# Performance work log

Measured on AMD Instinct MI355X. Metric: run time of the kernel, lower is better.

## Reference

```python
import jax, jax.numpy as jnp
import numpy as np

N_NODES = 50000
N_EDGES = 1600000
IN_DIM = 128
HID = 64
N_GRAPHS = 256


def gcn_conv(x, row, col, W, b, n_nodes):
    """PyG GCNConv: symmetric gcn_norm with self-loops, linear-then-aggregate."""
    h = x @ W  # [N, out]
    loop = jnp.arange(n_nodes, dtype=row.dtype)
    r = jnp.concatenate([row, loop])  # sources (messages from x[r])
    c = jnp.concatenate([col, loop])  # targets (aggregate at c)
    ew = jnp.ones(r.shape[0], dtype=x.dtype)
    deg = jax.ops.segment_sum(ew, c, num_segments=n_nodes)
    dinv = jnp.where(deg > 0, jax.lax.rsqrt(deg), 0.0).astype(x.dtype)
    norm = dinv[r] * dinv[c]  # [E+N]
    out = jax.ops.segment_sum(norm[:, None] * h[r], c, num_segments=n_nodes)
    return out + b


def global_mean_pool(x, batch, n_graphs):
    sums = jax.ops.segment_sum(x, batch, num_segments=n_graphs)
    cnt = jax.ops.segment_sum(jnp.ones(x.shape[0], x.dtype), batch, num_segments=n_graphs)
    return sums / jnp.clip(cnt, 1.0)[:, None]


def setup_inputs() -> dict:
    key = jax.random.key(0)
    ks = jax.random.split(key, 12)
    x = jax.random.normal(ks[0], (N_NODES, IN_DIM), dtype=jnp.float32)
    edge_index = jax.random.randint(ks[1], (2, N_EDGES), 0, N_NODES, dtype=jnp.int64)
    batch = jnp.sort(jax.random.randint(ks[2], (N_NODES,), 0, N_GRAPHS, dtype=jnp.int64))
    def glorot(k, shp):
        lim = float(np.sqrt(6.0 / (shp[0] + shp[1])))
        return jax.random.uniform(k, shp, jnp.float32, -lim, lim)
    return {
        "x": x,
        "edge_index": edge_index,
        "batch": batch,
        "W1": glorot(ks[3], (IN_DIM, HID)), "b1": jnp.zeros((HID,), jnp.float32),
        "W2": glorot(ks[4], (HID, HID)), "b2": jnp.zeros((HID,), jnp.float32),
        "W3": glorot(ks[5], (HID, HID)), "b3": jnp.zeros((HID,), jnp.float32),
        "Wl1": glorot(ks[6], (HID, 16)), "bl1": jnp.zeros((16,), jnp.float32),
        "Wl2": glorot(ks[7], (16, 1)), "bl2": jnp.zeros((1,), jnp.float32),
    }


def reference(x, edge_index, batch, W1, b1, W2, b2, W3, b3, Wl1, bl1, Wl2, bl2):
    n = x.shape[0]
    row, col = edge_index[0], edge_index[1]
    h = jax.nn.relu(gcn_conv(x, row, col, W1, b1, n))
    h = jax.nn.relu(gcn_conv(h, row, col, W2, b2, n))
    h = jax.nn.relu(gcn_conv(h, row, col, W3, b3, n))
    g = global_mean_pool(h, batch, N_GRAPHS)  # [G, 64]
    out = (g @ Wl1 + bl1) @ Wl2 + bl2  # [G, 1]
    return out
```

## Files before the change

kernel.cpp:

```cpp
#include <hip/hip_runtime.h>

#define HID 64
#define B1 512
#define NBMAX 200
#define CAP 10368
#define ENTCAP 3200
#define CPT 21
#define QBITS 3

typedef __attribute__((ext_vector_type(8))) short short8;
typedef __attribute__((ext_vector_type(4))) float float4v;
typedef float f32x2 __attribute__((ext_vector_type(2)));

__device__ __forceinline__ ushort f2bf(float f) {
  unsigned u = __float_as_uint(f);
  unsigned r = (u + 0x7fffu + ((u >> 16) & 1u)) >> 16;
  return (ushort)r;
}
__device__ __forceinline__ float bf2f(ushort v) {
  return __uint_as_float(((unsigned)v) << 16);
}

__device__ __forceinline__ void acc8(f32x2& a01, f32x2& a23, uint2 d) {
  f32x2 t0, t1;
  t0.x = __uint_as_float(d.x << 16);
  t0.y = __uint_as_float(d.x & 0xffff0000u);
  t1.x = __uint_as_float(d.y << 16);
  t1.y = __uint_as_float(d.y & 0xffff0000u);
  a01 += t0;
  a23 += t1;
}


__global__ __launch_bounds__(256) void bucket_hist(const int* __restrict__ col, int E, int epb,
                                                   int* __restrict__ blockcnt,
                                                   const float* __restrict__ W1,
                                                   ushort* __restrict__ Wt1h,
                                                   ushort* __restrict__ Wt1l) {
  int b = blockIdx.x, t = threadIdx.x;
  int gt = b * 256 + t;
  if (gt < 128 * 64) {
    int k = gt >> 6, nn = gt & 63;
    float w = W1[gt];
    ushort h = f2bf(w);
    Wt1h[nn * 128 + k] = h;
    Wt1l[nn * 128 + k] = f2bf(w - bf2f(h));
  }

  __shared__ int cnt[256];
  cnt[t] = 0;
  __syncthreads();
  int lo = b * epb, hi = min(lo + epb, E);
  int ecnt = hi - lo;
  if (ecnt > 0) {
    int ecnt4 = ecnt & ~3;
    for (int i = t * 4; i < ecnt4; i += 1024) {
      int4 c4 = *(const int4*)&col[lo + i];
      atomicAdd(&cnt[c4.x >> 8], 1);
      atomicAdd(&cnt[c4.y >> 8], 1);
      atomicAdd(&cnt[c4.z >> 8], 1);
      atomicAdd(&cnt[c4.w >> 8], 1);
    }
    for (int i = ecnt4 + t; i < ecnt; i += 256) atomicAdd(&cnt[col[lo + i] >> 8], 1);
  }
  __syncthreads();
  blockcnt[b * 256 + t] = cnt[t];
}

__global__ __launch_bounds__(512) void scan_blocks(int* __restrict__ blockcnt,
                                                   int* __restrict__ buckettot) {
  __shared__ int s[512];
  int k = blockIdx.x;
  int t = threadIdx.x;
  int v = blockcnt[t * 256 + k];
  s[t] = v;
  __syncthreads();
  for (int d = 1; d < 512; d <<= 1) {
    int u = (t >= d) ? s[t - d] : 0;
    __syncthreads();
    s[t] += u;
    __syncthreads();
  }
  blockcnt[t * 256 + k] = s[t] - v;
  if (t == 511) buckettot[k] = s[t];
}

__global__ __launch_bounds__(256) void scan_buckettot(const int* __restrict__ buckettot,
                                                      int* __restrict__ bucketbase,
                                                      int* __restrict__ csr_off, int n, int E,
                                                      int nb) {
  __shared__ int s[256];
  int t = threadIdx.x;
  int v = buckettot[t];
  s[t] = v;
  __syncthreads();
  for (int d = 1; d < 256; d <<= 1) {
    int u = (t >= d) ? s[t - d] : 0;
    __syncthreads();
    s[t] += u;
    __syncthreads();
  }
  bucketbase[t] = s[t] - v;
  if (t == 255) bucketbase[256] = s[255];
  if (t == 0) csr_off[n] = E;
}

__global__ __launch_bounds__(256) void bin_edges(const int* __restrict__ row,
                                                 const int* __restrict__ col, int E, int epb,
                                                 const int* __restrict__ blockcnt,
                                                 const int* __restrict__ bucketbase,
                                                 unsigned* __restrict__ binned) {
  __shared__ int cnt[256];
  __shared__ int ofs[256];
  __shared__ int gb[256];
  __shared__ int lcur[256];
  __shared__ unsigned ent[ENTCAP];
  __shared__ unsigned stage[ENTCAP];
  int b = blockIdx.x, t = threadIdx.x;
  int lo = b * epb, hi = min(lo + epb, E);
  int ecnt = hi - lo;

  cnt[t] = 0;
  __syncthreads();
  if (ecnt > 0) {
    int ecnt4 = ecnt & ~3;
    for (int i = t * 4; i < ecnt4; i += 1024) {
      int4 c4 = *(const int4*)&col[lo + i];
      int4 r4 = *(const int4*)&row[lo + i];
      uint4 e4;
      e4.x = ((unsigned)r4.x << 16) | (unsigned)c4.x;
      e4.y = ((unsigned)r4.y << 16) | (unsigned)c4.y;
      e4.z = ((unsigned)r4.z << 16) | (unsigned)c4.z;
      e4.w = ((unsigned)r4.w << 16) | (unsigned)c4.w;
      *(uint4*)&ent[i] = e4;
      atomicAdd(&cnt[c4.x >> 8], 1);
      atomicAdd(&cnt[c4.y >> 8], 1);
      atomicAdd(&cnt[c4.z >> 8], 1);
      atomicAdd(&cnt[c4.w >> 8], 1);
    }
    for (int i = ecnt4 + t; i < ecnt; i += 256) {
      int c = col[lo + i];
      int r = row[lo + i];
      ent[i] = ((unsigned)r << 16) | (unsigned)c;
      atomicAdd(&cnt[c >> 8], 1);
    }
  }
  __syncthreads();
  int v = cnt[t];
  ofs[t] = v;
  __syncthreads();
  for (int d = 1; d < 256; d <<= 1) {
    int u = (t >= d) ? ofs[t - d] : 0;
    __syncthreads();
    ofs[t] += u;
    __syncthreads();
  }
  int excl = ofs[t] - v;
  int g = bucketbase[t] + blockcnt[b * 256 + t];
  __syncthreads();
  ofs[t] = excl;
  gb[t] = g;
  lcur[t] = excl;
  __syncthreads();
  if (ecnt > 0) {
    for (int i = t; i < ecnt; i += 256) {
      unsigned en = ent[i];
      int p = atomicAdd(&lcur[(en >> 8) & 255], 1);
      stage[p] = en;
    }
  }
  __syncthreads();
  if (ecnt > 0) {
    for (int i = t; i < ecnt; i += 256) {
      unsigned en = stage[i];
      int bb = (en >> 8) & 255;
      binned[gb[bb] + (i - ofs[bb])] = en;
    }
  }
}

__global__ __launch_bounds__(512) void bucket_csr(const unsigned* __restrict__ binned,
                                                  const int* __restrict__ bucketbase,
                                                  int* __restrict__ csr_off,
                                                  int* __restrict__ csr_src,
                                                  float* __restrict__ dinv, int n) {
  __shared__ int cnt[256 << QBITS];
  __shared__ int sscan[512];
  __shared__ int lsrc[CAP];
  int k = blockIdx.x, t = threadIdx.x;
  int base = bucketbase[k], end = bucketbase[k + 1];
  int s = end - base;
  unsigned ent[CPT];
  cnt[t] = 0; cnt[512 + t] = 0; cnt[1024 + t] = 0; cnt[1536 + t] = 0;
  __syncthreads();
#pragma unroll
  for (int q = 0; q < CPT; ++q) {
    int i = q * 512 + t;
    if (i < s) {
      unsigned p = binned[base + i];
      ent[q] = p;
      atomicAdd(&cnt[((p & 255u) << QBITS) | ((p >> 29) & 7u)], 1);
    }
  }
  __syncthreads();
  int a0 = cnt[t * 4 + 0], a1 = cnt[t * 4 + 1], a2 = cnt[t * 4 + 2], a3 = cnt[t * 4 + 3];
  int tsum = a0 + a1 + a2 + a3;
  sscan[t] = tsum;
  __syncthreads();
  for (int d = 1; d < 512; d <<= 1) {
    int u = (t >= d) ? sscan[t - d] : 0;
    __syncthreads();
    sscan[t] += u;
    __syncthreads();
  }
  int ex = sscan[t] - tsum;
  cnt[t * 4 + 0] = ex;
  cnt[t * 4 + 1] = ex + a0;
  cnt[t * 4 + 2] = ex + a0 + a1;
  cnt[t * 4 + 3] = ex + a0 + a1 + a2;
  __syncthreads();
  if (t < 256) {
    int st = cnt[t << QBITS];
    int en2 = (t == 255) ? s : cnt[(t + 1) << QBITS];
    int node = (k << 8) + t;
    if (node < n) {
      csr_off[node] = base + st;
      dinv[node] = rsqrtf((float)(en2 - st + 1));
    }
  }
  __syncthreads();
#pragma unroll
  for (int q = 0; q < CPT; ++q) {
    int i = q * 512 + t;
    if (i < s) {
      unsigned p = ent[q];
      int pos = atomicAdd(&cnt[((p & 255u) << QBITS) | ((p >> 29) & 7u)], 1);
      if (pos < CAP) lsrc[pos] = (int)(p >> 16);
    }
  }
  __syncthreads();
  for (int i = t; i < s; i += 512) csr_src[base + i] = (i < CAP) ? lsrc[i] : 0;
}


template <int K>
__global__ __launch_bounds__(256) void gemm_mfma(const float* __restrict__ A,
                                                 const ushort* __restrict__ Wh,
                                                 const ushort* __restrict__ Wl,
                                                 const float* __restrict__ dinv,
                                                 ushort* __restrict__ out, int n) {
  int wave = (blockIdx.x * 256 + threadIdx.x) >> 6;
  int lane = threadIdx.x & 63;
  int row0 = wave * 16;
  if (row0 >= n) return;
  int m = lane & 15;
  int quad = lane >> 4;
  int r = row0 + m;
  int rc = (r < n) ? r : (n - 1);

  float4v acc[4];
#pragma unroll
  for (int t = 0; t < 4; ++t) acc[t] = (float4v){0.f, 0.f, 0.f, 0.f};

#pragma unroll
  for (int k0 = 0; k0 < K; k0 += 32) {
    const float4* xp = (const float4*)&A[(size_t)rc * K + k0 + quad * 8];
    float4 a0 = xp[0];
    float4 a1 = xp[1];
    float av[8] = {a0.x, a0.y, a0.z, a0.w, a1.x, a1.y, a1.z, a1.w};
    short8 ah, al;
#pragma unroll
    for (int i = 0; i < 8; ++i) {
      ushort h = f2bf(av[i]);
      ah[i] = (short)h;
      al[i] = (short)f2bf(av[i] - bf2f(h));
    }
#pragma unroll
    for (int t = 0; t < 4; ++t) {
      size_t wof = (size_t)(t * 16 + m) * K + k0 + quad * 8;
      short8 bh = *(const short8*)&Wh[wof];
      short8 bl = *(const short8*)&Wl[wof];
      acc[t] = __builtin_amdgcn_mfma_f32_16x16x32_bf16(ah, bh, acc[t], 0, 0, 0);
      acc[t] = __builtin_amdgcn_mfma_f32_16x16x32_bf16(al, bh, acc[t], 0, 0, 0);
      acc[t] = __builtin_amdgcn_mfma_f32_16x16x32_bf16(ah, bl, acc[t], 0, 0, 0);
    }
  }

  float4 dv = ((const float4*)dinv)[(row0 >> 2) + quad];
  float dvi[4] = {dv.x, dv.y, dv.z, dv.w};
#pragma unroll
  for (int i = 0; i < 4; ++i) {
    int orow = row0 + quad * 4 + i;
    if (orow < n) {
#pragma unroll
      for (int t = 0; t < 4; ++t) {
        out[(size_t)orow * 64 + t * 16 + m] = f2bf(dvi[i] * acc[t][i]);
      }
    }
  }
}


__global__ __launch_bounds__(256) void agg_gemm(
    const ushort* __restrict__ hs_in, const int* __restrict__ csr_off,
    const int* __restrict__ csr_src, const float* __restrict__ dinv,
    const float* __restrict__ bias, const float* __restrict__ W,
    ushort* __restrict__ hs_out, int n) {
  int wid = (blockIdx.x * 256 + threadIdx.x) >> 6;
  int lane = threadIdx.x & 63;
  if (wid >= n) return;
  int qe = lane >> 4;
  int fq = lane & 15;
  const uint2* hs2 = (const uint2*)hs_in;

  f32x2 a01 = {0.f, 0.f}, a23 = {0.f, 0.f};
  if (qe == 0) {
    acc8(a01, a23, hs2[(size_t)wid * 16 + fq]);
  }

  int j = csr_off[wid];
  int e = csr_off[wid + 1];

  int pre = min(e, (j + 3) & ~3);
  if (j + qe < pre) {
    int s0 = csr_src[j + qe];
    acc8(a01, a23, hs2[(size_t)s0 * 16 + fq]);
  }
  int base = pre;

  for (; base + 16 <= e; base += 16) {
    int4 s = *(const int4*)&csr_src[base + qe * 4];
    uint2 v0 = hs2[(size_t)s.x * 16 + fq];
    uint2 v1 = hs2[(size_t)s.y * 16 + fq];
    uint2 v2 = hs2[(size_t)s.z * 16 + fq];
    uint2 v3 = hs2[(size_t)s.w * 16 + fq];
    acc8(a01, a23, v0);
    acc8(a01, a23, v1);
    acc8(a01, a23, v2);
    acc8(a01, a23, v3);
  }

  for (; base + 4 <= e; base += 4) {
    int s0 = csr_src[base + qe];
    acc8(a01, a23, hs2[(size_t)s0 * 16 + fq]);
  }
  if (base + qe < e) {
    int s0 = csr_src[base + qe];
    acc8(a01, a23, hs2[(size_t)s0 * 16 + fq]);
  }

  a01.x += __shfl_xor(a01.x, 16, 64);
  a01.y += __shfl_xor(a01.y, 16, 64);
  a23.x += __shfl_xor(a23.x, 16, 64);
  a23.y += __shfl_xor(a23.y, 16, 64);
  a01.x += __shfl_xor(a01.x, 32, 64);
  a01.y += __shfl_xor(a01.y, 32, 64);
  a23.x += __shfl_xor(a23.x, 32, 64);
  a23.y += __shfl_xor(a23.y, 32, 64);

  float dd = dinv[wid];
  float4 bi = ((const float4*)bias)[fq];
  float r0 = fmaxf(dd * a01.x + bi.x, 0.f);
  float r1 = fmaxf(dd * a01.y + bi.y, 0.f);
  float r2 = fmaxf(dd * a23.x + bi.z, 0.f);
  float r3 = fmaxf(dd * a23.y + bi.w, 0.f);

  float h0 = 0.f, h1 = 0.f, h2 = 0.f, h3 = 0.f;
#pragma unroll
  for (int kq = 0; kq < 16; ++kq) {
    float f0 = __shfl(r0, kq, 64);
    float f1 = __shfl(r1, kq, 64);
    float f2 = __shfl(r2, kq, 64);
    float f3 = __shfl(r3, kq, 64);
    h0 += f0 * W[(kq * 4 + 0) * 64 + lane];
    h1 += f1 * W[(kq * 4 + 1) * 64 + lane];
    h2 += f2 * W[(kq * 4 + 2) * 64 + lane];
    h3 += f3 * W[(kq * 4 + 3) * 64 + lane];
  }
  float h = (h0 + h1) + (h2 + h3);
  hs_out[(size_t)wid * 64 + lane] = f2bf(dd * h);
}


__global__ __launch_bounds__(256) void agg_kernel(
    const ushort* __restrict__ hs, const int* __restrict__ csr_off,
    const int* __restrict__ csr_src, const float* __restrict__ dinv,
    const float* __restrict__ bias, float* __restrict__ out, int n) {
  int wid = (blockIdx.x * 256 + threadIdx.x) >> 6;
  int lane = threadIdx.x & 63;
  if (wid >= n) return;
  int qe = lane >> 4;
  int fq = lane & 15;
  const uint2* hs2 = (const uint2*)hs;

  f32x2 a01 = {0.f, 0.f}, a23 = {0.f, 0.f};
  if (qe == 0) {
    acc8(a01, a23, hs2[(size_t)wid * 16 + fq]);
  }

  int j = csr_off[wid];
  int e = csr_off[wid + 1];

  int pre = min(e, (j + 3) & ~3);
  if (j + qe < pre) {
    int s0 = csr_src[j + qe];
    acc8(a01, a23, hs2[(size_t)s0 * 16 + fq]);
  }
  int base = pre;

  for (; base + 16 <= e; base += 16) {
    int4 s = *(const int4*)&csr_src[base + qe * 4];
    uint2 v0 = hs2[(size_t)s.x * 16 + fq];
    uint2 v1 = hs2[(size_t)s.y * 16 + fq];
    uint2 v2 = hs2[(size_t)s.z * 16 + fq];
    uint2 v3 = hs2[(size_t)s.w * 16 + fq];
    acc8(a01, a23, v0);
    acc8(a01, a23, v1);
    acc8(a01, a23, v2);
    acc8(a01, a23, v3);
  }

  for (; base + 4 <= e; base += 4) {
    int s0 = csr_src[base + qe];
    acc8(a01, a23, hs2[(size_t)s0 * 16 + fq]);
  }
  if (base + qe < e) {
    int s0 = csr_src[base + qe];
    acc8(a01, a23, hs2[(size_t)s0 * 16 + fq]);
  }

  a01.x += __shfl_xor(a01.x, 16, 64);
  a01.y += __shfl_xor(a01.y, 16, 64);
  a23.x += __shfl_xor(a23.x, 16, 64);
  a23.y += __shfl_xor(a23.y, 16, 64);
  a01.x += __shfl_xor(a01.x, 32, 64);
  a01.y += __shfl_xor(a01.y, 32, 64);
  a23.x += __shfl_xor(a23.x, 32, 64);
  a23.y += __shfl_xor(a23.y, 32, 64);

  if (qe == 0) {
    float d = dinv[wid];
    float4 bi = ((const float4*)bias)[fq];
    float4 r;
    r.x = fmaxf(d * a01.x + bi.x, 0.f);
    r.y = fmaxf(d * a01.y + bi.y, 0.f);
    r.z = fmaxf(d * a23.x + bi.z, 0.f);
    r.w = fmaxf(d * a23.y + bi.w, 0.f);
    ((float4*)out)[(size_t)wid * 16 + fq] = r;
  }
}


__global__ __launch_bounds__(256) void pool_mlp_kernel(
    const float* __restrict__ a, const int* __restrict__ batch, int n,
    const float* __restrict__ Wl1, const float* __restrict__ bl1,
    const float* __restrict__ Wl2, const float* __restrict__ bl2,
    float* __restrict__ out) {
  int g = blockIdx.x;
  int t = threadIdx.x;
  int lane = t & 63;
  int w = t >> 6;

  int lo = 0, hi = n;
  while (lo < hi) {
    int m = (lo + hi) >> 1;
    if (batch[m] < g) lo = m + 1; else hi = m;
  }
  int start = lo;
  lo = start; hi = n;
  while (lo < hi) {
    int m = (lo + hi) >> 1;
    if (batch[m] < g + 1) lo = m + 1; else hi = m;
  }
  int end = lo;

  float s = 0.f;
  for (int i = start + w; i < end; i += 4) s += a[i * 64 + lane];

  __shared__ float ps[4][64];
  __shared__ float gv[64];
  __shared__ float hv[16];
  ps[w][lane] = s;
  __syncthreads();
  if (w == 0) {
    float tot = ps[0][lane] + ps[1][lane] + ps[2][lane] + ps[3][lane];
    gv[lane] = tot / (float)max(end - start, 1);
  }
  __syncthreads();
  if (t < 16) {
    float h = bl1[t];
    for (int k = 0; k < 64; ++k) h += gv[k] * Wl1[k * 16 + t];
    hv[t] = h;
  }
  __syncthreads();
  if (t == 0) {
    float o = bl2[0];
    for (int j2 = 0; j2 < 16; ++j2) o += hv[j2] * Wl2[j2];
    out[g] = o;
  }
}


extern "C" void kernel_launch(void* const* d_in, const int* in_sizes, int n_in,
                              void* d_out, int out_size, void* d_ws, size_t ws_size,
                              hipStream_t stream) {
  const float* x = (const float*)d_in[0];
  const int* ei = (const int*)d_in[1];
  const int* batch = (const int*)d_in[2];
  const float* W1 = (const float*)d_in[3];
  const float* b1 = (const float*)d_in[4];
  const float* W2 = (const float*)d_in[5];
  const float* b2 = (const float*)d_in[6];
  const float* W3 = (const float*)d_in[7];
  const float* b3 = (const float*)d_in[8];
  const float* Wl1 = (const float*)d_in[9];
  const float* bl1 = (const float*)d_in[10];
  const float* Wl2 = (const float*)d_in[11];
  const float* bl2 = (const float*)d_in[12];

  int n = in_sizes[0] / 128;
  int E = in_sizes[1] / 2;
  int G = out_size;
  int nb = (n + 255) >> 8;
  int epb = (((E + B1 - 1) / B1) + 15) & ~15;

  const int* row = ei;
  const int* col = ei + E;

  char* p = (char*)d_ws;
  int* blockcnt = (int*)p;    p += B1 * 256 * 4;
  int* buckettot = (int*)p;   p += 256 * 4;
  int* bucketbase = (int*)p;  p += 272 * 4;
  int* csr_off = (int*)p;     p += 50064 * 4;
  float* dinv = (float*)p;    p += 50016 * 4;
  ushort* Wt1h = (ushort*)p;  p += 128 * 64 * 2;
  ushort* Wt1l = (ushort*)p;  p += 128 * 64 * 2;
  int* csr_src = (int*)p;     p += (size_t)((E + 15) / 16 * 16) * 4;
  ushort* hs_a = (ushort*)p;  p += (size_t)n * 64 * 2;
  ushort* hs_b = (ushort*)p;  p += (size_t)n * 64 * 2;
  float* abuf = (float*)p;
  unsigned* binned = (unsigned*)hs_a;

  bucket_hist<<<B1, 256, 0, stream>>>(col, E, epb, blockcnt, W1, Wt1h, Wt1l);
  scan_blocks<<<256, 512, 0, stream>>>(blockcnt, buckettot);
  scan_buckettot<<<1, 256, 0, stream>>>(buckettot, bucketbase, csr_off, n, E, nb);
  bin_edges<<<B1, 256, 0, stream>>>(row, col, E, epb, blockcnt, bucketbase, binned);
  bucket_csr<<<nb, 512, 0, stream>>>(binned, bucketbase, csr_off, csr_src, dinv, n);

  int nwaves = (n + 15) / 16;
  int gblocks = (nwaves + 3) / 4;
  int ablocks = (n * 64 + 255) / 256;

  gemm_mfma<128><<<gblocks, 256, 0, stream>>>(x, Wt1h, Wt1l, dinv, hs_a, n);
  agg_gemm<<<ablocks, 256, 0, stream>>>(hs_a, csr_off, csr_src, dinv, b1, W2, hs_b, n);
  agg_gemm<<<ablocks, 256, 0, stream>>>(hs_b, csr_off, csr_src, dinv, b2, W3, hs_a, n);
  agg_kernel<<<ablocks, 256, 0, stream>>>(hs_a, csr_off, csr_src, dinv, b3, abuf, n);
  pool_mlp_kernel<<<G, 256, 0, stream>>>(abuf, batch, n, Wl1, bl1, Wl2, bl2, (float*)d_out);
}
```

Baseline: 300.8 us.

## Fold bucket-total scan into consumers and use persistent grid-stride aggregation

Removes the single-block scan_buckettot launch. bin_edges and bucket_csr now each recompute the 256-entry prefix sum of bucket totals in shared memory, and bucket_csr block 0 writes csr_off[n]. The aggregation kernels switch from one wave per node across about 12500 blocks to a fixed grid of 2048 blocks that loop over nodes with a grid stride, and the bias load is hoisted out of the loop. The aim is to cut launch and dependency overhead and the cost of block scheduling, in exchange for redundant scan work in every block and possibly less latency hiding in the gather.

Result: slower. 337.1 us (+12.1%).

```diff
diff --git a/kernel.cpp b/kernel.cpp
--- a/kernel.cpp
+++ b/kernel.cpp
@@ -2,11 +2,11 @@
 
 #define HID 64
 #define B1 512
-#define NBMAX 200
 #define CAP 10368
 #define ENTCAP 3200
 #define CPT 21
 #define QBITS 3
+#define AGGB 2048
 
 typedef __attribute__((ext_vector_type(8))) short short8;
 typedef __attribute__((ext_vector_type(4))) float float4v;
@@ -85,30 +85,10 @@
   if (t == 511) buckettot[k] = s[t];
 }
 
-__global__ __launch_bounds__(256) void scan_buckettot(const int* __restrict__ buckettot,
-                                                      int* __restrict__ bucketbase,
-                                                      int* __restrict__ csr_off, int n, int E,
-                                                      int nb) {
-  __shared__ int s[256];
-  int t = threadIdx.x;
-  int v = buckettot[t];
-  s[t] = v;
-  __syncthreads();
-  for (int d = 1; d < 256; d <<= 1) {
-    int u = (t >= d) ? s[t - d] : 0;
-    __syncthreads();
-    s[t] += u;
-    __syncthreads();
-  }
-  bucketbase[t] = s[t] - v;
-  if (t == 255) bucketbase[256] = s[255];
-  if (t == 0) csr_off[n] = E;
-}
-
 __global__ __launch_bounds__(256) void bin_edges(const int* __restrict__ row,
                                                  const int* __restrict__ col, int E, int epb,
                                                  const int* __restrict__ blockcnt,
-                                                 const int* __restrict__ bucketbase,
+                                                 const int* __restrict__ buckettot,
                                                  unsigned* __restrict__ binned) {
   __shared__ int cnt[256];
   __shared__ int ofs[256];
@@ -119,6 +99,18 @@
   int b = blockIdx.x, t = threadIdx.x;
   int lo = b * epb, hi = min(lo + epb, E);
   int ecnt = hi - lo;
+
+  int bt = buckettot[t];
+  ofs[t] = bt;
+  __syncthreads();
+  for (int d = 1; d < 256; d <<= 1) {
+    int u = (t >= d) ? ofs[t - d] : 0;
+    __syncthreads();
+    ofs[t] += u;
+    __syncthreads();
+  }
+  int bb = ofs[t] - bt;
+  __syncthreads();
 
   cnt[t] = 0;
   __syncthreads();
@@ -156,7 +148,7 @@
     __syncthreads();
   }
   int excl = ofs[t] - v;
-  int g = bucketbase[t] + blockcnt[b * 256 + t];
+  int g = bb + blockcnt[b * 256 + t];
   __syncthreads();
   ofs[t] = excl;
   gb[t] = g;
@@ -173,14 +165,14 @@
   if (ecnt > 0) {
     for (int i = t; i < ecnt; i += 256) {
       unsigned en = stage[i];
-      int bb = (en >> 8) & 255;
-      binned[gb[bb] + (i - ofs[bb])] = en;
+      int bk = (en >> 8) & 255;
+      binned[gb[bk] + (i - ofs[bk])] = en;
     }
   }
 }
 
 __global__ __launch_bounds__(512) void bucket_csr(const unsigned* __restrict__ binned,
-                                                  const int* __restrict__ bucketbase,
+                                                  const int* __restrict__ buckettot,
                                                   int* __restrict__ csr_off,
                                                   int* __restrict__ csr_src,
                                                   float* __restrict__ dinv, int n) {
@@ -188,7 +180,21 @@
   __shared__ int sscan[512];
   __shared__ int lsrc[CAP];
   int k = blockIdx.x, t = threadIdx.x;
-  int base = bucketbase[k], end = bucketbase[k + 1];
+
+  int tot = (t < 256) ? buckettot[t] : 0;
+  sscan[t] = tot;
+  __syncthreads();
+  for (int d = 1; d < 512; d <<= 1) {
+    int u = (t >= d) ? sscan[t - d] : 0;
+    __syncthreads();
+    sscan[t] += u;
+    __syncthreads();
+  }
+  int base = (k == 0) ? 0 : sscan[k - 1];
+  int end = sscan[k];
+  if (k == 0 && t == 0) csr_off[n] = sscan[255];
+  __syncthreads();
+
   int s = end - base;
   unsigned ent[CPT];
   cnt[t] = 0; cnt[512 + t] = 0; cnt[1024 + t] = 0; cnt[1536 + t] = 0;
@@ -306,79 +312,81 @@
     const int* __restrict__ csr_src, const float* __restrict__ dinv,
     const float* __restrict__ bias, const float* __restrict__ W,
     ushort* __restrict__ hs_out, int n) {
-  int wid = (blockIdx.x * 256 + threadIdx.x) >> 6;
   int lane = threadIdx.x & 63;
-  if (wid >= n) return;
   int qe = lane >> 4;
   int fq = lane & 15;
   const uint2* hs2 = (const uint2*)hs_in;
-
-  f32x2 a01 = {0.f, 0.f}, a23 = {0.f, 0.f};
-  if (qe == 0) {
-    acc8(a01, a23, hs2[(size_t)wid * 16 + fq]);
-  }
-
-  int j = csr_off[wid];
-  int e = csr_off[wid + 1];
-
-  int pre = min(e, (j + 3) & ~3);
-  if (j + qe < pre) {
-    int s0 = csr_src[j + qe];
-    acc8(a01, a23, hs2[(size_t)s0 * 16 + fq]);
-  }
-  int base = pre;
-
-  for (; base + 16 <= e; base += 16) {
-    int4 s = *(const int4*)&csr_src[base + qe * 4];
-    uint2 v0 = hs2[(size_t)s.x * 16 + fq];
-    uint2 v1 = hs2[(size_t)s.y * 16 + fq];
-    uint2 v2 = hs2[(size_t)s.z * 16 + fq];
-    uint2 v3 = hs2[(size_t)s.w * 16 + fq];
-    acc8(a01, a23, v0);
-    acc8(a01, a23, v1);
-    acc8(a01, a23, v2);
-    acc8(a01, a23, v3);
-  }
-
-  for (; base + 4 <= e; base += 4) {
-    int s0 = csr_src[base + qe];
-    acc8(a01, a23, hs2[(size_t)s0 * 16 + fq]);
-  }
-  if (base + qe < e) {
-    int s0 = csr_src[base + qe];
-    acc8(a01, a23, hs2[(size_t)s0 * 16 + fq]);
-  }
-
-  a01.x += __shfl_xor(a01.x, 16, 64);
-  a01.y += __shfl_xor(a01.y, 16, 64);
-  a23.x += __shfl_xor(a23.x, 16, 64);
-  a23.y += __shfl_xor(a23.y, 16, 64);
-  a01.x += __shfl_xor(a01.x, 32, 64);
-  a01.y += __shfl_xor(a01.y, 32, 64);
-  a23.x += __shfl_xor(a23.x, 32, 64);
-  a23.y += __shfl_xor(a23.y, 32, 64);
-
-  float dd = dinv[wid];
   float4 bi = ((const float4*)bias)[fq];
-  float r0 = fmaxf(dd * a01.x + bi.x, 0.f);
-  float r1 = fmaxf(dd * a01.y + bi.y, 0.f);
-  float r2 = fmaxf(dd * a23.x + bi.z, 0.f);
-  float r3 = fmaxf(dd * a23.y + bi.w, 0.f);
-
-  float h0 = 0.f, h1 = 0.f, h2 = 0.f, h3 = 0.f;
-#pragma unroll
-  for (int kq = 0; kq < 16; ++kq) {
-    float f0 = __shfl(r0, kq, 64);
-    float f1 = __shfl(r1, kq, 64);
-    float f2 = __shfl(r2, kq, 64);
-    float f3 = __shfl(r3, kq, 64);
-    h0 += f0 * W[(kq * 4 + 0) * 64 + lane];
-    h1 += f1 * W[(kq * 4 + 1) * 64 + lane];
-    h2 += f2 * W[(kq * 4 + 2) * 64 + lane];
-    h3 += f3 * W[(kq * 4 + 3) * 64 + lane];
-  }
-  float h = (h0 + h1) + (h2 + h3);
-  hs_out[(size_t)wid * 64 + lane] = f2bf(dd * h);
+  int wslot = (blockIdx.x * 256 + threadIdx.x) >> 6;
+  int gw = (AGGB * 256) >> 6;
+
+  for (int wid = wslot; wid < n; wid += gw) {
+    f32x2 a01 = {0.f, 0.f}, a23 = {0.f, 0.f};
+    if (qe == 0) {
+      acc8(a01, a23, hs2[(size_t)wid * 16 + fq]);
+    }
+
+    int j = csr_off[wid];
+    int e = csr_off[wid + 1];
+
+    int pre = min(e, (j + 3) & ~3);
+    if (j + qe < pre) {
+      int s0 = csr_src[j + qe];
+      acc8(a01, a23, hs2[(size_t)s0 * 16 + fq]);
+    }
+    int base = pre;
+
+    for (; base + 16 <= e; base += 16) {
+      int4 s = *(const int4*)&csr_src[base + qe * 4];
+      uint2 v0 = hs2[(size_t)s.x * 16 + fq];
+      uint2 v1 = hs2[(size_t)s.y * 16 + fq];
+      uint2 v2 = hs2[(size_t)s.z * 16 + fq];
+      uint2 v3 = hs2[(size_t)s.w * 16 + fq];
+      acc8(a01, a23, v0);
+      acc8(a01, a23, v1);
+      acc8(a01, a23, v2);
+      acc8(a01, a23, v3);
+    }
+
+    for (; base + 4 <= e; base += 4) {
+      int s0 = csr_src[base + qe];
+      acc8(a01, a23, hs2[(size_t)s0 * 16 + fq]);
+    }
+    if (base + qe < e) {
+      int s0 = csr_src[base + qe];
+      acc8(a01, a23, hs2[(size_t)s0 * 16 + fq]);
+    }
+
+    a01.x += __shfl_xor(a01.x, 16, 64);
+    a01.y += __shfl_xor(a01.y, 16, 64);
+    a23.x += __shfl_xor(a23.x, 16, 64);
+    a23.y += __shfl_xor(a23.y, 16, 64);
+    a01.x += __shfl_xor(a01.x, 32, 64);
+    a01.y += __shfl_xor(a01.y, 32, 64);
+    a23.x += __shfl_xor(a23.x, 32, 64);
+    a23.y += __shfl_xor(a23.y, 32, 64);
+
+    float dd = dinv[wid];
+    float r0 = fmaxf(dd * a01.x + bi.x, 0.f);
+    float r1 = fmaxf(dd * a01.y + bi.y, 0.f);
+    float r2 = fmaxf(dd * a23.x + bi.z, 0.f);
+    float r3 = fmaxf(dd * a23.y + bi.w, 0.f);
+
+    float h0 = 0.f, h1 = 0.f, h2 = 0.f, h3 = 0.f;
+#pragma unroll
+    for (int kq = 0; kq < 16; ++kq) {
+      float f0 = __shfl(r0, kq, 64);
+      float f1 = __shfl(r1, kq, 64);
+      float f2 = __shfl(r2, kq, 64);
+      float f3 = __shfl(r3, kq, 64);
+      h0 += f0 * W[(kq * 4 + 0) * 64 + lane];
+      h1 += f1 * W[(kq * 4 + 1) * 64 + lane];
+      h2 += f2 * W[(kq * 4 + 2) * 64 + lane];
+      h3 += f3 * W[(kq * 4 + 3) * 64 + lane];
+    }
+    float h = (h0 + h1) + (h2 + h3);
+    hs_out[(size_t)wid * 64 + lane] = f2bf(dd * h);
+  }
 }
 
 
@@ -386,67 +394,69 @@
     const ushort* __restrict__ hs, const int* __restrict__ csr_off,
     const int* __restrict__ csr_src, const float* __restrict__ dinv,
     const float* __restrict__ bias, float* __restrict__ out, int n) {
-  int wid = (blockIdx.x * 256 + threadIdx.x) >> 6;
   int lane = threadIdx.x & 63;
-  if (wid >= n) return;
   int qe = lane >> 4;
   int fq = lane & 15;
   const uint2* hs2 = (const uint2*)hs;
-
-  f32x2 a01 = {0.f, 0.f}, a23 = {0.f, 0.f};
-  if (qe == 0) {
-    acc8(a01, a23, hs2[(size_t)wid * 16 + fq]);
-  }
-
-  int j = csr_off[wid];
-  int e = csr_off[wid + 1];
-
-  int pre = min(e, (j + 3) & ~3);
-  if (j + qe < pre) {
-    int s0 = csr_src[j + qe];
-    acc8(a01, a23, hs2[(size_t)s0 * 16 + fq]);
-  }
-  int base = pre;
-
-  for (; base + 16 <= e; base += 16) {
-    int4 s = *(const int4*)&csr_src[base + qe * 4];
-    uint2 v0 = hs2[(size_t)s.x * 16 + fq];
-    uint2 v1 = hs2[(size_t)s.y * 16 + fq];
-    uint2 v2 = hs2[(size_t)s.z * 16 + fq];
-    uint2 v3 = hs2[(size_t)s.w * 16 + fq];
-    acc8(a01, a23, v0);
-    acc8(a01, a23, v1);
-    acc8(a01, a23, v2);
-    acc8(a01, a23, v3);
-  }
-
-  for (; base + 4 <= e; base += 4) {
-    int s0 = csr_src[base + qe];
-    acc8(a01, a23, hs2[(size_t)s0 * 16 + fq]);
-  }
-  if (base + qe < e) {
-    int s0 = csr_src[base + qe];
-    acc8(a01, a23, hs2[(size_t)s0 * 16 + fq]);
-  }
-
-  a01.x += __shfl_xor(a01.x, 16, 64);
-  a01.y += __shfl_xor(a01.y, 16, 64);
-  a23.x += __shfl_xor(a23.x, 16, 64);
-  a23.y += __shfl_xor(a23.y, 16, 64);
-  a01.x += __shfl_xor(a01.x, 32, 64);
-  a01.y += __shfl_xor(a01.y, 32, 64);
-  a23.x += __shfl_xor(a23.x, 32, 64);
-  a23.y += __shfl_xor(a23.y, 32, 64);
-
-  if (qe == 0) {
-    float d = dinv[wid];
-    float4 bi = ((const float4*)bias)[fq];
-    float4 r;
-    r.x = fmaxf(d * a01.x + bi.x, 0.f);
-    r.y = fmaxf(d * a01.y + bi.y, 0.f);
-    r.z = fmaxf(d * a23.x + bi.z, 0.f);
-    r.w = fmaxf(d * a23.y + bi.w, 0.f);
-    ((float4*)out)[(size_t)wid * 16 + fq] = r;
+  float4 bi = ((const float4*)bias)[fq];
+  int wslot = (blockIdx.x * 256 + threadIdx.x) >> 6;
+  int gw = (AGGB * 256) >> 6;
+
+  for (int wid = wslot; wid < n; wid += gw) {
+    f32x2 a01 = {0.f, 0.f}, a23 = {0.f, 0.f};
+    if (qe == 0) {
+      acc8(a01, a23, hs2[(size_t)wid * 16 + fq]);
+    }
+
+    int j = csr_off[wid];
+    int e = csr_off[wid + 1];
+
+    int pre = min(e, (j + 3) & ~3);
+    if (j + qe < pre) {
+      int s0 = csr_src[j + qe];
+      acc8(a01, a23, hs2[(size_t)s0 * 16 + fq]);
+    }
+    int base = pre;
+
+    for (; base + 16 <= e; base += 16) {
+      int4 s = *(const int4*)&csr_src[base + qe * 4];
+      uint2 v0 = hs2[(size_t)s.x * 16 + fq];
+      uint2 v1 = hs2[(size_t)s.y * 16 + fq];
+      uint2 v2 = hs2[(size_t)s.z * 16 + fq];
+      uint2 v3 = hs2[(size_t)s.w * 16 + fq];
+      acc8(a01, a23, v0);
+      acc8(a01, a23, v1);
+      acc8(a01, a23, v2);
+      acc8(a01, a23, v3);
+    }
+
+    for (; base + 4 <= e; base += 4) {
+      int s0 = csr_src[base + qe];
+      acc8(a01, a23, hs2[(size_t)s0 * 16 + fq]);
+    }
+    if (base + qe < e) {
+      int s0 = csr_src[base + qe];
+      acc8(a01, a23, hs2[(size_t)s0 * 16 + fq]);
+    }
+
+    a01.x += __shfl_xor(a01.x, 16, 64);
+    a01.y += __shfl_xor(a01.y, 16, 64);
+    a23.x += __shfl_xor(a23.x, 16, 64);
+    a23.y += __shfl_xor(a23.y, 16, 64);
+    a01.x += __shfl_xor(a01.x, 32, 64);
+    a01.y += __shfl_xor(a01.y, 32, 64);
+    a23.x += __shfl_xor(a23.x, 32, 64);
+    a23.y += __shfl_xor(a23.y, 32, 64);
+
+    if (qe == 0) {
+      float d = dinv[wid];
+      float4 r;
+      r.x = fmaxf(d * a01.x + bi.x, 0.f);
+      r.y = fmaxf(d * a01.y + bi.y, 0.f);
+      r.z = fmaxf(d * a23.x + bi.z, 0.f);
+      r.w = fmaxf(d * a23.y + bi.w, 0.f);
+      ((float4*)out)[(size_t)wid * 16 + fq] = r;
+    }
   }
 }
 
@@ -530,7 +540,6 @@
   char* p = (char*)d_ws;
   int* blockcnt = (int*)p;    p += B1 * 256 * 4;
   int* buckettot = (int*)p;   p += 256 * 4;
-  int* bucketbase = (int*)p;  p += 272 * 4;
   int* csr_off = (int*)p;     p += 50064 * 4;
   float* dinv = (float*)p;    p += 50016 * 4;
   ushort* Wt1h = (ushort*)p;  p += 128 * 64 * 2;
@@ -543,17 +552,15 @@
 
   bucket_hist<<<B1, 256, 0, stream>>>(col, E, epb, blockcnt, W1, Wt1h, Wt1l);
   scan_blocks<<<256, 512, 0, stream>>>(blockcnt, buckettot);
-  scan_buckettot<<<1, 256, 0, stream>>>(buckettot, bucketbase, csr_off, n, E, nb);
-  bin_edges<<<B1, 256, 0, stream>>>(row, col, E, epb, blockcnt, bucketbase, binned);
-  bucket_csr<<<nb, 512, 0, stream>>>(binned, bucketbase, csr_off, csr_src, dinv, n);
+  bin_edges<<<B1, 256, 0, stream>>>(row, col, E, epb, blockcnt, buckettot, binned);
+  bucket_csr<<<nb, 512, 0, stream>>>(binned, buckettot, csr_off, csr_src, dinv, n);
 
   int nwaves = (n + 15) / 16;
   int gblocks = (nwaves + 3) / 4;
-  int ablocks = (n * 64 + 255) / 256;
 
   gemm_mfma<128><<<gblocks, 256, 0, stream>>>(x, Wt1h, Wt1l, dinv, hs_a, n);
-  agg_gemm<<<ablocks, 256, 0, stream>>>(hs_a, csr_off, csr_src, dinv, b1, W2, hs_b, n);
-  agg_gemm<<<ablocks, 256, 0, stream>>>(hs_b, csr_off, csr_src, dinv, b2, W3, hs_a, n);
-  agg_kernel<<<ablocks, 256, 0, stream>>>(hs_a, csr_off, csr_src, dinv, b3, abuf, n);
+  agg_gemm<<<AGGB, 256, 0, stream>>>(hs_a, csr_off, csr_src, dinv, b1, W2, hs_b, n);
+  agg_gemm<<<AGGB, 256, 0, stream>>>(hs_b, csr_off, csr_src, dinv, b2, W3, hs_a, n);
+  agg_kernel<<<AGGB, 256, 0, stream>>>(hs_a, csr_off, csr_src, dinv, b3, abuf, n);
   pool_mlp_kernel<<<G, 256, 0, stream>>>(abuf, batch, n, Wl1, bl1, Wl2, bl2, (float*)d_out);
 }
```
